# Kernel optimization log

Measured on AMD Instinct MI355X. Metric: run time of the kernel, lower is better.

The kernel has to match this reference:

```python
import jax, jax.numpy as jnp
import numpy as np

B, N = 2, 8192

PARAM_SHAPES = {
    'down0_w': (32, 3), 'down0_b': (32,),
    'sc1_w1': (32, 35), 'sc1_b1': (32,), 'sc1_w2': (64, 32), 'sc1_b2': (64,),
    'sc2_w1': (64, 67), 'sc2_b1': (64,), 'sc2_w2': (128, 64), 'sc2_b2': (128,),
    'sc3_w1': (128, 131), 'sc3_b1': (128,), 'sc3_w2': (192, 128), 'sc3_b2': (192,),
    'sc4_w1': (192, 195), 'sc4_b1': (192,), 'sc4_w2': (192, 192), 'sc4_b2': (192,),
    'up4_w1': (192, 195), 'up4_b1': (192,), 'up4_w2': (192, 384), 'up4_b2': (192,),
    'up3_w1': (128, 195), 'up3_b1': (128,), 'up3_w2': (128, 256), 'up3_b2': (128,),
    'up2_w1': (64, 131), 'up2_b1': (64,), 'up2_w2': (64, 128), 'up2_b2': (64,),
    'up1_w1': (32, 67), 'up1_b1': (32,), 'up1_w2': (32, 64), 'up1_b2': (32,),
}
PNAMES = list(PARAM_SHAPES.keys())


def _fps(xyz, m):
    # xyz [N,3] -> [m] int32 farthest-point-sample indices (deterministic, start at point 0)
    def body(dmin, _):
        nxt = jnp.argmax(dmin)
        d = jnp.sum((xyz - xyz[nxt]) ** 2, -1)
        return jnp.minimum(dmin, d), nxt.astype(jnp.int32)
    d0 = jnp.sum((xyz - xyz[0]) ** 2, -1)
    _, rest = jax.lax.scan(body, d0, None, length=m - 1)
    return jnp.concatenate([jnp.zeros((1,), jnp.int32), rest])


def _gather(pts, idx):
    # pts [B,N,C], idx [B,...] -> [B,...,C]
    return jax.vmap(lambda p, i: p[i])(pts, idx)


def _ball_query(new_xyz, xyz, radius, k):
    # first-k points within radius, invalid slots filled with the first valid index
    d2 = jnp.sum((new_xyz[:, :, None, :] - xyz[:, None, :, :]) ** 2, -1)  # [B,M,N]
    n = xyz.shape[1]
    order = jnp.where(d2 <= radius * radius, jnp.arange(n)[None, None, :], n)
    idx = jnp.argsort(order, axis=-1)[..., :k]
    valid = jnp.take_along_axis(order, idx, -1) < n
    return jnp.where(valid, idx, idx[..., :1])


def _knn(query, ref, k):
    d2 = jnp.sum((query[:, :, None, :] - ref[:, None, :, :]) ** 2, -1)  # [B,Nq,Nr]
    _, idx = jax.lax.top_k(-d2, k)
    return idx


def _mlp(h, w, b):
    # pointwise shared MLP layer with ReLU on channel-last tensor
    return jax.nn.relu(jnp.einsum('...c,oc->...o', h, w) + b)


def _set_conv(xyz, feat, npoint, radius, k, w1, b1, w2, b2):
    # PointNet++-style SetConv: FPS -> ball-query group -> shared MLP -> max-pool
    fps_idx = jax.vmap(_fps, (0, None))(xyz, npoint)          # [B,M]
    new_xyz = _gather(xyz, fps_idx)                            # [B,M,3]
    gi = _ball_query(new_xyz, xyz, radius, k)                  # [B,M,k]
    h = jnp.concatenate([_gather(xyz, gi) - new_xyz[:, :, None, :], _gather(feat, gi)], -1)
    h = _mlp(_mlp(h, w1, b1), w2, b2)                          # [B,M,k,Cout]
    return new_xyz, fps_idx, jnp.max(h, axis=2)


def _set_upconv(s_xyz, d_xyz, s_feat, d_feat, k, w1, b1, w2, b2):
    # FlowNet3D-style SetUpConv: kNN from dense to sparse -> MLP -> max-pool -> fuse with dense feat
    gi = _knn(d_xyz, s_xyz, k)                                 # [B,Nd,k]
    h = jnp.concatenate([_gather(s_xyz, gi) - d_xyz[:, :, None, :], _gather(s_feat, gi)], -1)
    pooled = jnp.max(_mlp(h, w1, b1), axis=2)                  # [B,Nd,m1]
    return _mlp(jnp.concatenate([pooled, d_feat], -1), w2, b2)


def _encoder(pc, feat, p):
    xyz = jnp.transpose(pc, (0, 2, 1))                         # [B,N,3]
    f0 = _mlp(jnp.transpose(feat, (0, 2, 1)), p['down0_w'], p['down0_b'])  # [B,N,32]
    xyz1, i1, f1 = _set_conv(xyz, f0, 2048, 0.5, 16, p['sc1_w1'], p['sc1_b1'], p['sc1_w2'], p['sc1_b2'])
    xyz2, i2, f2 = _set_conv(xyz1, f1, 512, 1.0, 16, p['sc2_w1'], p['sc2_b1'], p['sc2_w2'], p['sc2_b2'])
    xyz3, i3, f3 = _set_conv(xyz2, f2, 128, 2.0, 16, p['sc3_w1'], p['sc3_b1'], p['sc3_w2'], p['sc3_b2'])
    xyz4, i4, f4 = _set_conv(xyz3, f3, 64, 4.0, 16, p['sc4_w1'], p['sc4_b1'], p['sc4_w2'], p['sc4_b2'])
    u3 = _set_upconv(xyz4, xyz3, f4, f3, 8, p['up4_w1'], p['up4_b1'], p['up4_w2'], p['up4_b2'])
    u2 = _set_upconv(xyz3, xyz2, u3, f2, 8, p['up3_w1'], p['up3_b1'], p['up3_w2'], p['up3_b2'])
    u1 = _set_upconv(xyz2, xyz1, u2, f1, 8, p['up2_w1'], p['up2_b1'], p['up2_w2'], p['up2_b2'])
    u0 = _set_upconv(xyz1, xyz, u1, f0, 8, p['up1_w1'], p['up1_b1'], p['up1_w2'], p['up1_b2'])
    return (xyz1, xyz2, xyz3), (i1, i2, i3), (u0, u1, u2, u3)


def setup_inputs() -> dict:
    key = jax.random.key(0)
    ks = jax.random.split(key, 2 + len(PNAMES))
    inp = {
        'pc': jax.random.normal(ks[0], (B, 3, N), jnp.float32),
        'feat': jax.random.normal(ks[1], (B, 3, N), jnp.float32),
    }
    for i, name in enumerate(PNAMES):
        inp[name] = jax.random.normal(ks[2 + i], PARAM_SHAPES[name], jnp.float32) * 0.05
    return inp


def reference(pc, feat, down0_w, down0_b, sc1_w1, sc1_b1, sc1_w2, sc1_b2, sc2_w1, sc2_b1, sc2_w2, sc2_b2, sc3_w1, sc3_b1, sc3_w2, sc3_b2, sc4_w1, sc4_b1, sc4_w2, sc4_b2, up4_w1, up4_b1, up4_w2, up4_b2, up3_w1, up3_b1, up3_w2, up3_b2, up2_w1, up2_b1, up2_w2, up2_b2, up1_w1, up1_b1, up1_w2, up1_b2):
    # GenFlow_unit.forward with gts[0] is None -> pure encoder path
    loc = locals()
    p = {k: loc[k] for k in PNAMES}
    (x1, x2, x3), (i1, i2, i3), (u0, u1, u2, u3) = _encoder(pc, feat, p)
    t = lambda a: jnp.transpose(a, (0, 2, 1))  # back to torch channel-first convention
    return (t(x1), t(x2), t(x3), i1, i2, i3, t(u0), t(u1), t(u2), t(u3))
```

## Files before the change

### kernel.cpp

```cpp
#include <hip/hip_runtime.h>
#include <hip/hip_bf16.h>
#include <cstdint>

#define DEV __device__ __forceinline__

typedef float f32x2 __attribute__((ext_vector_type(2)));

DEV float sqdist(float ax, float ay, float az, float bx, float by, float bz) {
    float dx = __fsub_rn(ax, bx), dy = __fsub_rn(ay, by), dz = __fsub_rn(az, bz);
    return __fadd_rn(__fadd_rn(__fmul_rn(dx, dx), __fmul_rn(dy, dy)), __fmul_rn(dz, dz));
}

DEV f32x2 sqdist2(f32x2 ax, f32x2 ay, f32x2 az, float bx, float by, float bz) {
#pragma clang fp contract(off)
    f32x2 dx = ax - bx, dy = ay - by, dz = az - bz;
    return (dx * dx + dy * dy) + dz * dz;
}

DEV unsigned short f2bf(float f) {
    unsigned int u = __float_as_uint(f);
    u += 0x7fffu + ((u >> 16) & 1u);
    return (unsigned short)(u >> 16);
}

DEV float bf2f(unsigned short u) { return __uint_as_float(((unsigned int)u) << 16); }

template <int CTRL>
DEV int dpp_i(int v) { return __builtin_amdgcn_update_dpp(v, v, CTRL, 0xf, 0xf, false); }
template <int CTRL>
DEV float dpp_f(float v) { return __int_as_float(dpp_i<CTRL>(__float_as_int(v))); }

enum : int {
    O_X1 = 0, O_X2 = 12288, O_X3 = 15360,
    O_I1 = 16128, O_I2 = 20224, O_I3 = 21248,
    O_U0 = 21504, O_U1 = 545792, O_U2 = 807936, O_U3 = 939008
};

__global__ __launch_bounds__(256) void k_init(const float* __restrict__ pc,
                                              const float* __restrict__ feat,
                                              const float* __restrict__ w0,
                                              const float* __restrict__ b0,
                                              float* __restrict__ xyz,
                                              unsigned short* __restrict__ f0) {
    const int N = 8192;
    int i = blockIdx.x * blockDim.x + threadIdx.x;
    if (i >= 2 * N) return;
    int b = i / N, n = i % N;
    float fx0 = feat[(b * 3 + 0) * N + n];
    float fx1 = feat[(b * 3 + 1) * N + n];
    float fx2 = feat[(b * 3 + 2) * N + n];
    xyz[i * 3 + 0] = pc[(b * 3 + 0) * N + n];
    xyz[i * 3 + 1] = pc[(b * 3 + 1) * N + n];
    xyz[i * 3 + 2] = pc[(b * 3 + 2) * N + n];
#pragma unroll
    for (int o = 0; o < 32; o++) {
        float acc = b0[o];
        acc = fmaf(w0[o * 3 + 0], fx0, acc);
        acc = fmaf(w0[o * 3 + 1], fx1, acc);
        acc = fmaf(w0[o * 3 + 2], fx2, acc);
        f0[(size_t)i * 32 + o] = f2bf(fmaxf(acc, 0.f));
    }
}

template <int N, int M, int T>
DEV void fps_body(int b, int t, const float* __restrict__ xyz,
                  int* __restrict__ idx_out, char* smem) {
    constexpr int P = N / T;
    constexpr int P2 = P / 2;
    constexpr int W = T / 64;
    const float* X = xyz + (size_t)b * N * 3;
    float* sx = (float*)smem;
    float* sy = sx + N;
    float* sz = sy + N;
    unsigned long long* skey = (unsigned long long*)(smem + 12 * N);
    f32x2 px[P2], py[P2], pz[P2], dmin[P2];
    float c0x = X[0], c0y = X[1], c0z = X[2];
#pragma unroll
    for (int i = 0; i < P2; i++) {
        int p0 = (2 * i) * T + t, p1 = (2 * i + 1) * T + t;
        px[i] = f32x2{X[p0 * 3 + 0], X[p1 * 3 + 0]};
        py[i] = f32x2{X[p0 * 3 + 1], X[p1 * 3 + 1]};
        pz[i] = f32x2{X[p0 * 3 + 2], X[p1 * 3 + 2]};
        sx[p0] = px[i].x; sy[p0] = py[i].x; sz[p0] = pz[i].x;
        sx[p1] = px[i].y; sy[p1] = py[i].y; sz[p1] = pz[i].y;
        dmin[i] = sqdist2(px[i], py[i], pz[i], c0x, c0y, c0z);
    }
    if (t == 0) {
        idx_out[b * M] = 0;
        skey[0] = 0; skey[1] = 0; skey[2] = 0;
    }
    __syncthreads();
    int jm = 1;
    for (int j = 1; j < M; j++) {
        f32x2 m2[P2];
#pragma unroll
        for (int i = 0; i < P2; i++) m2[i] = dmin[i];
#pragma unroll
        for (int s = P2 / 2; s >= 1; s >>= 1)
#pragma unroll
            for (int i = 0; i < s; i++) m2[i] = __builtin_elementwise_max(m2[i], m2[i + s]);
        float bv = fmaxf(m2[0].x, m2[0].y);
        int ii[P];
#pragma unroll
        for (int i = 0; i < P; i++)
            ii[i] = (dmin[i >> 1][i & 1] == bv) ? (i * T + t) : 0x7fffffff;
#pragma unroll
        for (int s = P / 2; s >= 1; s >>= 1)
#pragma unroll
            for (int i = 0; i < s; i++) ii[i] = min(ii[i], ii[i + s]);
        int bi = ii[0];
        float bw = bv;
        bw = fmaxf(bw, dpp_f<0x121>(bw));
        bw = fmaxf(bw, dpp_f<0x122>(bw));
        bw = fmaxf(bw, dpp_f<0x124>(bw));
        bw = fmaxf(bw, dpp_f<0x128>(bw));
        bw = fmaxf(bw, dpp_f<0x142>(bw));
        bw = fmaxf(bw, dpp_f<0x143>(bw));
        float bvw = __int_as_float(__builtin_amdgcn_readlane(__float_as_int(bw), 63));
        unsigned int im = (bv == bvw) ? (unsigned int)bi : 0xffffffffu;
        im = min(im, (unsigned int)dpp_i<0x121>((int)im));
        im = min(im, (unsigned int)dpp_i<0x122>((int)im));
        im = min(im, (unsigned int)dpp_i<0x124>((int)im));
        im = min(im, (unsigned int)dpp_i<0x128>((int)im));
        im = min(im, (unsigned int)dpp_i<0x142>((int)im));
        im = min(im, (unsigned int)dpp_i<0x143>((int)im));
        int biw = __builtin_amdgcn_readlane((int)im, 63);
        int gi;
        if constexpr (W > 1) {
            unsigned long long key =
                ((unsigned long long)__float_as_uint(bvw) << 32) | (unsigned int)~biw;
            if ((t & 63) == 0) atomicMax(&skey[jm], key);
            __syncthreads();
            unsigned long long gk = skey[jm];
            gi = (int)~(unsigned int)gk;
            if (t == 0) skey[jm == 0 ? 2 : jm - 1] = 0;
            jm = (jm == 2) ? 0 : jm + 1;
        } else {
            gi = biw;
        }
        if (t == 0) idx_out[b * M + j] = gi;
        float cx = sx[gi], cy = sy[gi], cz = sz[gi];
#pragma unroll
        for (int i = 0; i < P2; i++)
            dmin[i] = __builtin_elementwise_min(
                dmin[i], sqdist2(px[i], py[i], pz[i], cx, cy, cz));
    }
}

template <int N, int M, int T>
__global__ __launch_bounds__(T, 1) void k_fps(const float* __restrict__ xyz,
                                              int* __restrict__ idx_out) {
    __shared__ __align__(16) char smem[12 * N + 24];
    fps_body<N, M, T>(blockIdx.x, threadIdx.x, xyz, idx_out, smem);
}

__global__ __launch_bounds__(256) void k_gather(const float* __restrict__ xyz_src,
                                                const int* __restrict__ idx,
                                                float* __restrict__ xyz_dst,
                                                int NS, int M) {
    int i = blockIdx.x * blockDim.x + threadIdx.x;
    if (i >= 2 * M) return;
    int b = i / M;
    int id = idx[i] & (NS - 1);
    xyz_dst[i * 3 + 0] = xyz_src[((size_t)b * NS + id) * 3 + 0];
    xyz_dst[i * 3 + 1] = xyz_src[((size_t)b * NS + id) * 3 + 1];
    xyz_dst[i * 3 + 2] = xyz_src[((size_t)b * NS + id) * 3 + 2];
}

template <int NS, int CF, int CMID, int COUT>
DEV void setconv_body(int q, int bb, int tid, int bdim,
                      const float* __restrict__ X, const unsigned short* __restrict__ F,
                      const float* __restrict__ C, const float* __restrict__ w1,
                      const float* __restrict__ b1, const float* __restrict__ w2,
                      const float* __restrict__ b2, unsigned short* __restrict__ fout,
                      float r2, int M, char* smem) {
    constexpr int CIN = 3 + CF;
    constexpr int K = 16;
    constexpr int M8 = CMID / 8;
    constexpr int O8 = COUT / 8;
    int blk = bb * M + q;
    const float* Xb = X + (size_t)bb * NS * 3;
    const unsigned short* Fb = F + (size_t)bb * NS * CF;
    int* s_n = (int*)smem;
    int* s_cntp = (int*)(smem + 64);
    float* s_h = (float*)(smem + 80);
    float* s_mid = s_h + K * CIN;
    float* s_pool = s_mid + K * CMID;
    float cx = C[(size_t)blk * 3 + 0], cy = C[(size_t)blk * 3 + 1], cz = C[(size_t)blk * 3 + 2];
    if (tid < 64) {
        int lane = tid;
        int cnt = 0;
        for (int base = 0; base < NS; base += 64) {
            int p = base + lane;
            float d2 = sqdist(Xb[p * 3], Xb[p * 3 + 1], Xb[p * 3 + 2], cx, cy, cz);
            bool in = (d2 <= r2);
            unsigned long long msk = __ballot(in);
            if (in) {
                int pos = cnt + __popcll(msk & ((1ull << lane) - 1ull));
                if (pos < K) s_n[pos] = p;
            }
            cnt += __popcll(msk);
            if (cnt >= K) break;
        }
        if (lane == 0) *s_cntp = cnt < K ? cnt : K;
    }
    __syncthreads();
    int cnt = *s_cntp;
    if (tid >= cnt && tid < K) s_n[tid] = s_n[0];
    __syncthreads();
    for (int tIdx = tid; tIdx < K * CIN; tIdx += bdim) {
        int n = tIdx / CIN, c = tIdx % CIN;
        int gi = s_n[n];
        float v;
        if (c < 3) v = __fsub_rn(Xb[gi * 3 + c], (c == 0 ? cx : (c == 1 ? cy : cz)));
        else v = bf2f(Fb[(size_t)gi * CF + (c - 3)]);
        s_h[n * CIN + c] = v;
    }
    __syncthreads();
    if (tid < 128) {
        int n = tid >> 3, sub = tid & 7;
#pragma unroll
        for (int j = 0; j < M8; j++) {
            int m = sub * M8 + j;
            float acc = b1[m];
#pragma unroll 4
            for (int c = 0; c < CIN; c++) acc = fmaf(w1[m * CIN + c], s_h[n * CIN + c], acc);
            s_mid[n * CMID + m] = fmaxf(acc, 0.f);
        }
    }
    __syncthreads();
    if (tid < 128) {
        int n = tid >> 3, sub = tid & 7;
        float vals[O8];
#pragma unroll
        for (int j = 0; j < O8; j++) {
            int o = sub * O8 + j;
            float acc = b2[o];
#pragma unroll 4
            for (int c = 0; c < CMID; c++) acc = fmaf(w2[o * CMID + c], s_mid[n * CMID + c], acc);
            vals[j] = fmaxf(acc, 0.f);
        }
#pragma unroll
        for (int j = 0; j < O8; j++) {
            vals[j] = fmaxf(vals[j], __shfl_xor(vals[j], 8, 64));
            vals[j] = fmaxf(vals[j], __shfl_xor(vals[j], 16, 64));
            vals[j] = fmaxf(vals[j], __shfl_xor(vals[j], 32, 64));
        }
        int lw = tid & 63, wv = tid >> 6;
        if (lw < 8) {
#pragma unroll
            for (int j = 0; j < O8; j++) s_pool[wv * COUT + lw * O8 + j] = vals[j];
        }
    }
    __syncthreads();
    if (tid < 8) {
#pragma unroll
        for (int j = 0; j < O8; j++) {
            int o = tid * O8 + j;
            fout[(size_t)blk * COUT + o] = f2bf(fmaxf(s_pool[o], s_pool[COUT + o]));
        }
    }
}

template <int NS, int CF, int CMID, int COUT>
__global__ __launch_bounds__(128) void k_setconv(
    const float* __restrict__ X, const unsigned short* __restrict__ F,
    const float* __restrict__ C, const float* __restrict__ w1,
    const float* __restrict__ b1, const float* __restrict__ w2,
    const float* __restrict__ b2, unsigned short* __restrict__ fout,
    float r2, int M) {
    constexpr int K = 16;
    constexpr int CIN = 3 + CF;
    __shared__ __align__(16) char smem[80 + 4 * (K * CIN + K * CMID + 2 * COUT)];
    setconv_body<NS, CF, CMID, COUT>(blockIdx.x, blockIdx.y, threadIdx.x, blockDim.x,
                                     X, F, C, w1, b1, w2, b2, fout, r2, M, smem);
}

template <int N, int M, int T, int NS, int CF, int CMID, int COUT>
__global__ __launch_bounds__(T, 1) void k_fps_sc(
    const float* __restrict__ fxyz, int* __restrict__ idx_out,
    const float* __restrict__ X, const unsigned short* __restrict__ F,
    const float* __restrict__ C, const float* __restrict__ w1,
    const float* __restrict__ b1, const float* __restrict__ w2,
    const float* __restrict__ b2, unsigned short* __restrict__ fout,
    float r2, int Msc) {
    constexpr int K = 16;
    constexpr int CIN = 3 + CF;
    constexpr int FPS_B = 12 * N + 24;
    constexpr int SC_B = 80 + 4 * (K * CIN + K * CMID + 2 * COUT);
    constexpr int SB = FPS_B > SC_B ? FPS_B : SC_B;
    __shared__ __align__(16) char smem[SB];
    if (blockIdx.x < 2) {
        fps_body<N, M, T>(blockIdx.x, threadIdx.x, fxyz, idx_out, smem);
    } else {
        int lin = blockIdx.x - 2;
        int q = lin % Msc, bb = lin / Msc;
        setconv_body<NS, CF, CMID, COUT>(q, bb, threadIdx.x, blockDim.x,
                                         X, F, C, w1, b1, w2, b2, fout, r2, Msc, smem);
    }
}

template <int S, int CS, int CMID, int CD, int COUT, bool TRANS>
__global__ __launch_bounds__(64) void k_upconv(
    const float* __restrict__ SX, const float* __restrict__ DX,
    const void* __restrict__ SFv, const unsigned short* __restrict__ DF,
    const float* __restrict__ w1, const float* __restrict__ b1,
    const float* __restrict__ w2, const float* __restrict__ b2,
    float* __restrict__ out, int o_off, int ND) {
    constexpr int K = 8;
    constexpr int CIN = 3 + CS;
    constexpr int CIN2 = CMID + CD;
    constexpr int M8 = CMID / 8;
    int q = blockIdx.x, b = blockIdx.y;
    int blk = b * ND + q;
    int lane = threadIdx.x;
    const float* SXb = SX + (size_t)b * S * 3;
    float qx = DX[(size_t)blk * 3], qy = DX[(size_t)blk * 3 + 1], qz = DX[(size_t)blk * 3 + 2];
    __shared__ int s_k[K];
    __shared__ float s_h[K][CIN];
    __shared__ float s_in2[CIN2];
    float bd[K];
    int bi[K];
#pragma unroll
    for (int i = 0; i < K; i++) { bd[i] = 3.0e38f; bi[i] = 0x7fffffff; }
    for (int p = lane; p < S; p += 64) {
        float d2 = sqdist(SXb[p * 3], SXb[p * 3 + 1], SXb[p * 3 + 2], qx, qy, qz);
        if (d2 < bd[K - 1] || (d2 == bd[K - 1] && p < bi[K - 1])) {
            bd[K - 1] = d2; bi[K - 1] = p;
#pragma unroll
            for (int j = K - 1; j > 0; j--) {
                bool sw = (bd[j] < bd[j - 1]) || (bd[j] == bd[j - 1] && bi[j] < bi[j - 1]);
                if (sw) {
                    float tv = bd[j]; bd[j] = bd[j - 1]; bd[j - 1] = tv;
                    int ti = bi[j]; bi[j] = bi[j - 1]; bi[j - 1] = ti;
                }
            }
        }
    }
    for (int r = 0; r < K; r++) {
        float vv = bd[0];
        float bw = vv;
        bw = fminf(bw, dpp_f<0x121>(bw));
        bw = fminf(bw, dpp_f<0x122>(bw));
        bw = fminf(bw, dpp_f<0x124>(bw));
        bw = fminf(bw, dpp_f<0x128>(bw));
        bw = fminf(bw, dpp_f<0x142>(bw));
        bw = fminf(bw, dpp_f<0x143>(bw));
        float vw = __int_as_float(__builtin_amdgcn_readlane(__float_as_int(bw), 63));
        unsigned int im = (vv == vw) ? (unsigned int)bi[0] : 0xffffffffu;
        im = min(im, (unsigned int)dpp_i<0x121>((int)im));
        im = min(im, (unsigned int)dpp_i<0x122>((int)im));
        im = min(im, (unsigned int)dpp_i<0x124>((int)im));
        im = min(im, (unsigned int)dpp_i<0x128>((int)im));
        im = min(im, (unsigned int)dpp_i<0x142>((int)im));
        im = min(im, (unsigned int)dpp_i<0x143>((int)im));
        int iw = __builtin_amdgcn_readlane((int)im, 63);
        if (lane == 0) s_k[r] = iw;
        if (iw == bi[0]) {
#pragma unroll
            for (int j = 0; j < K - 1; j++) { bd[j] = bd[j + 1]; bi[j] = bi[j + 1]; }
            bd[K - 1] = 3.0e38f; bi[K - 1] = 0x7fffffff;
        }
    }
    __syncthreads();
    for (int tIdx = lane; tIdx < K * CIN; tIdx += 64) {
        int n = tIdx / CIN, c = tIdx % CIN;
        int gi = s_k[n];
        float v;
        if (c < 3) v = __fsub_rn(SXb[gi * 3 + c], (c == 0 ? qx : (c == 1 ? qy : qz)));
        else if (TRANS) v = ((const float*)SFv)[((size_t)b * CS + (c - 3)) * S + gi];
        else v = bf2f(((const unsigned short*)SFv)[((size_t)b * S + gi) * CS + (c - 3)]);
        s_h[n][c] = v;
    }
    for (int c = lane; c < CD; c += 64) s_in2[CMID + c] = bf2f(DF[(size_t)blk * CD + c]);
    __syncthreads();
    int n = lane >> 3, sub = lane & 7;
    float vals[M8];
#pragma unroll
    for (int j = 0; j < M8; j++) {
        int m = sub * M8 + j;
        float acc = b1[m];
#pragma unroll 4
        for (int c = 0; c < CIN; c++) acc = fmaf(w1[m * CIN + c], s_h[n][c], acc);
        vals[j] = fmaxf(acc, 0.f);
    }
#pragma unroll
    for (int j = 0; j < M8; j++) {
        vals[j] = fmaxf(vals[j], __shfl_xor(vals[j], 8, 64));
        vals[j] = fmaxf(vals[j], __shfl_xor(vals[j], 16, 64));
        vals[j] = fmaxf(vals[j], __shfl_xor(vals[j], 32, 64));
    }
    if (lane < 8) {
#pragma unroll
        for (int j = 0; j < M8; j++) s_in2[lane * M8 + j] = vals[j];
    }
    __syncthreads();
    for (int o = lane; o < COUT; o += 64) {
        float acc = b2[o];
#pragma unroll 4
        for (int c = 0; c < CIN2; c++) acc = fmaf(w2[o * CIN2 + c], s_in2[c], acc);
        out[o_off + ((size_t)b * COUT + o) * ND + q] = fmaxf(acc, 0.f);
    }
}

__global__ __launch_bounds__(256) void k_finalize(
    const float* __restrict__ xyz1, const float* __restrict__ xyz2,
    const float* __restrict__ xyz3, const int* __restrict__ idx1,
    const int* __restrict__ idx2, const int* __restrict__ idx3,
    float* __restrict__ out) {
    int i = blockIdx.x * blockDim.x + threadIdx.x;
    const float* xs;
    const int* is;
    int M, ox, oi, j;
    if (i < 4096) { xs = xyz1; is = idx1; M = 2048; ox = O_X1; oi = O_I1; j = i; }
    else if (i < 5120) { xs = xyz2; is = idx2; M = 512; ox = O_X2; oi = O_I2; j = i - 4096; }
    else if (i < 5376) { xs = xyz3; is = idx3; M = 128; ox = O_X3; oi = O_I3; j = i - 5120; }
    else return;
    int b = j / M, m = j % M;
    out[ox + (b * 3 + 0) * M + m] = xs[j * 3 + 0];
    out[ox + (b * 3 + 1) * M + m] = xs[j * 3 + 1];
    out[ox + (b * 3 + 2) * M + m] = xs[j * 3 + 2];
    out[oi + j] = (float)is[j];
}

extern "C" void kernel_launch(void* const* d_in, const int* in_sizes, int n_in,
                              void* d_out, int out_size, void* d_ws, size_t ws_size,
                              hipStream_t stream) {
    const float* pc = (const float*)d_in[0];
    const float* feat = (const float*)d_in[1];
    const float* w0 = (const float*)d_in[2];
    const float* b0v = (const float*)d_in[3];
    const float* sc1w1 = (const float*)d_in[4];  const float* sc1b1 = (const float*)d_in[5];
    const float* sc1w2 = (const float*)d_in[6];  const float* sc1b2 = (const float*)d_in[7];
    const float* sc2w1 = (const float*)d_in[8];  const float* sc2b1 = (const float*)d_in[9];
    const float* sc2w2 = (const float*)d_in[10]; const float* sc2b2 = (const float*)d_in[11];
    const float* sc3w1 = (const float*)d_in[12]; const float* sc3b1 = (const float*)d_in[13];
    const float* sc3w2 = (const float*)d_in[14]; const float* sc3b2 = (const float*)d_in[15];
    const float* sc4w1 = (const float*)d_in[16]; const float* sc4b1 = (const float*)d_in[17];
    const float* sc4w2 = (const float*)d_in[18]; const float* sc4b2 = (const float*)d_in[19];
    const float* up4w1 = (const float*)d_in[20]; const float* up4b1 = (const float*)d_in[21];
    const float* up4w2 = (const float*)d_in[22]; const float* up4b2 = (const float*)d_in[23];
    const float* up3w1 = (const float*)d_in[24]; const float* up3b1 = (const float*)d_in[25];
    const float* up3w2 = (const float*)d_in[26]; const float* up3b2 = (const float*)d_in[27];
    const float* up2w1 = (const float*)d_in[28]; const float* up2b1 = (const float*)d_in[29];
    const float* up2w2 = (const float*)d_in[30]; const float* up2b2 = (const float*)d_in[31];
    const float* up1w1 = (const float*)d_in[32]; const float* up1b1 = (const float*)d_in[33];
    const float* up1w2 = (const float*)d_in[34]; const float* up1b2 = (const float*)d_in[35];
    float* out = (float*)d_out;

    char* ws = (char*)d_ws;
    size_t off = 0;
    auto A = [&](size_t bytes) -> char* {
        char* p = ws + off;
        off += (bytes + 255) & ~(size_t)255;
        return p;
    };
    float* xyz  = (float*)A((size_t)2 * 8192 * 3 * 4);
    int* idx1   = (int*)A((size_t)2 * 2048 * 4);
    int* idx2   = (int*)A((size_t)2 * 512 * 4);
    int* idx3   = (int*)A((size_t)2 * 128 * 4);
    int* idx4   = (int*)A((size_t)2 * 64 * 4);
    float* xyz1 = (float*)A((size_t)2 * 2048 * 3 * 4);
    float* xyz2 = (float*)A((size_t)2 * 512 * 3 * 4);
    float* xyz3 = (float*)A((size_t)2 * 128 * 3 * 4);
    float* xyz4 = (float*)A((size_t)2 * 64 * 3 * 4);
    unsigned short* f0 = (unsigned short*)A((size_t)2 * 8192 * 32 * 2);
    unsigned short* f1 = (unsigned short*)A((size_t)2 * 2048 * 64 * 2);
    unsigned short* f2 = (unsigned short*)A((size_t)2 * 512 * 128 * 2);
    unsigned short* f3 = (unsigned short*)A((size_t)2 * 128 * 192 * 2);
    unsigned short* f4 = (unsigned short*)A((size_t)2 * 64 * 192 * 2);

    k_init<<<(2 * 8192 + 255) / 256, 256, 0, stream>>>(pc, feat, w0, b0v, xyz, f0);

    k_fps<8192, 2048, 512><<<2, 512, 0, stream>>>(xyz, idx1);
    k_gather<<<16, 256, 0, stream>>>(xyz, idx1, xyz1, 8192, 2048);
    k_fps_sc<2048, 512, 512, 8192, 32, 32, 64><<<2 + 2 * 2048, 512, 0, stream>>>(
        xyz1, idx2, xyz, f0, xyz1, sc1w1, sc1b1, sc1w2, sc1b2, f1, 0.25f, 2048);
    k_gather<<<4, 256, 0, stream>>>(xyz1, idx2, xyz2, 2048, 512);
    k_fps_sc<512, 128, 256, 2048, 64, 64, 128><<<2 + 2 * 512, 256, 0, stream>>>(
        xyz2, idx3, xyz1, f1, xyz2, sc2w1, sc2b1, sc2w2, sc2b2, f2, 1.0f, 512);
    k_gather<<<1, 256, 0, stream>>>(xyz2, idx3, xyz3, 512, 128);
    k_fps<128, 64, 64><<<2, 64, 0, stream>>>(xyz3, idx4);
    k_gather<<<1, 128, 0, stream>>>(xyz3, idx4, xyz4, 128, 64);
    k_setconv<512, 128, 128, 192><<<dim3(128, 2), 128, 0, stream>>>(
        xyz2, f2, xyz3, sc3w1, sc3b1, sc3w2, sc3b2, f3, 4.0f, 128);
    k_setconv<128, 192, 192, 192><<<dim3(64, 2), 128, 0, stream>>>(
        xyz3, f3, xyz4, sc4w1, sc4b1, sc4w2, sc4b2, f4, 16.0f, 64);

    k_upconv<64, 192, 192, 192, 192, false><<<dim3(128, 2), 64, 0, stream>>>(
        xyz4, xyz3, f4, f3, up4w1, up4b1, up4w2, up4b2, out, O_U3, 128);
    k_upconv<128, 192, 128, 128, 128, true><<<dim3(512, 2), 64, 0, stream>>>(
        xyz3, xyz2, out + O_U3, f2, up3w1, up3b1, up3w2, up3b2, out, O_U2, 512);
    k_upconv<512, 128, 64, 64, 64, true><<<dim3(2048, 2), 64, 0, stream>>>(
        xyz2, xyz1, out + O_U2, f1, up2w1, up2b1, up2w2, up2b2, out, O_U1, 2048);
    k_upconv<2048, 64, 32, 32, 32, true><<<dim3(8192, 2), 64, 0, stream>>>(
        xyz1, xyz, out + O_U1, f0, up1w1, up1b1, up1w2, up1b2, out, O_U0, 8192);

    k_finalize<<<(5376 + 255) / 256, 256, 0, stream>>>(
        xyz1, xyz2, xyz3, idx1, idx2, idx3, out);
}
```

Measured before the change: 3.846 ms.

## Spatially bin points and prune first-level FPS updates with per-thread bounding boxes

```diff
diff --git a/kernel.cpp b/kernel.cpp
--- a/kernel.cpp
+++ b/kernel.cpp
@@ -59,6 +59,181 @@
         acc = fmaf(w0[o * 3 + 1], fx1, acc);
         acc = fmaf(w0[o * 3 + 2], fx2, acc);
         f0[(size_t)i * 32 + o] = f2bf(fmaxf(acc, 0.f));
+    }
+}
+
+template <int N, int T>
+__global__ __launch_bounds__(T) void k_bin(const float* __restrict__ xyz,
+                                           float* __restrict__ xp, float* __restrict__ yp,
+                                           float* __restrict__ zp, int* __restrict__ pid) {
+    constexpr int W = T / 64;
+    int b = blockIdx.x, t = threadIdx.x;
+    const float* X = xyz + (size_t)b * N * 3;
+    __shared__ float smn[3][W], smx[3][W];
+    __shared__ int hist[512], scan[512], cnt[512];
+    float mn[3] = {3e38f, 3e38f, 3e38f}, mx[3] = {-3e38f, -3e38f, -3e38f};
+    for (int p = t; p < N; p += T) {
+        float v[3] = {X[p * 3], X[p * 3 + 1], X[p * 3 + 2]};
+#pragma unroll
+        for (int a = 0; a < 3; a++) { mn[a] = fminf(mn[a], v[a]); mx[a] = fmaxf(mx[a], v[a]); }
+    }
+#pragma unroll
+    for (int a = 0; a < 3; a++) {
+#pragma unroll
+        for (int m = 1; m < 64; m <<= 1) {
+            mn[a] = fminf(mn[a], __shfl_xor(mn[a], m, 64));
+            mx[a] = fmaxf(mx[a], __shfl_xor(mx[a], m, 64));
+        }
+    }
+    if ((t & 63) == 0) {
+#pragma unroll
+        for (int a = 0; a < 3; a++) { smn[a][t >> 6] = mn[a]; smx[a][t >> 6] = mx[a]; }
+    }
+    for (int i = t; i < 512; i += T) { hist[i] = 0; cnt[i] = 0; }
+    __syncthreads();
+#pragma unroll
+    for (int a = 0; a < 3; a++) {
+        mn[a] = smn[a][0]; mx[a] = smx[a][0];
+#pragma unroll
+        for (int w = 1; w < W; w++) { mn[a] = fminf(mn[a], smn[a][w]); mx[a] = fmaxf(mx[a], smx[a][w]); }
+    }
+    float inv[3];
+#pragma unroll
+    for (int a = 0; a < 3; a++) inv[a] = 8.0f / fmaxf(mx[a] - mn[a], 1e-9f);
+    auto bin_of = [&](float x, float y, float z) {
+        int ix = min(7, max(0, (int)((x - mn[0]) * inv[0])));
+        int iy = min(7, max(0, (int)((y - mn[1]) * inv[1])));
+        int iz = min(7, max(0, (int)((z - mn[2]) * inv[2])));
+        return (ix << 6) | (iy << 3) | iz;
+    };
+    for (int p = t; p < N; p += T) {
+        atomicAdd(&hist[bin_of(X[p * 3], X[p * 3 + 1], X[p * 3 + 2])], 1);
+    }
+    __syncthreads();
+    if (t < 512) scan[t] = hist[t];
+    __syncthreads();
+    for (int s = 1; s < 512; s <<= 1) {
+        int v = 0;
+        if (t < 512 && t >= s) v = scan[t - s];
+        __syncthreads();
+        if (t < 512) scan[t] += v;
+        __syncthreads();
+    }
+    for (int p = t; p < N; p += T) {
+        float x = X[p * 3], y = X[p * 3 + 1], z = X[p * 3 + 2];
+        int bid = bin_of(x, y, z);
+        int pos = (scan[bid] - hist[bid]) + atomicAdd(&cnt[bid], 1);
+        xp[(size_t)b * N + pos] = x;
+        yp[(size_t)b * N + pos] = y;
+        zp[(size_t)b * N + pos] = z;
+        pid[(size_t)b * N + pos] = p;
+    }
+}
+
+template <int N, int M, int T>
+__global__ __launch_bounds__(T, 1) void k_fps_pruned(
+    const float* __restrict__ xp, const float* __restrict__ yp,
+    const float* __restrict__ zp, const int* __restrict__ pidg,
+    const float* __restrict__ xyz, int* __restrict__ idx_out) {
+    constexpr int P = N / T;
+    constexpr int P2 = P / 2;
+    int b = blockIdx.x, t = threadIdx.x;
+    const float* XP = xp + (size_t)b * N;
+    const float* YP = yp + (size_t)b * N;
+    const float* ZP = zp + (size_t)b * N;
+    const int* PIDG = pidg + (size_t)b * N;
+    __shared__ float sx[N], sy[N], sz[N];
+    __shared__ int spid[N];
+    __shared__ unsigned long long skey[3];
+    f32x2 px[P2], py[P2], pz[P2], dmin[P2];
+    float c0x = xyz[(size_t)b * N * 3 + 0];
+    float c0y = xyz[(size_t)b * N * 3 + 1];
+    float c0z = xyz[(size_t)b * N * 3 + 2];
+    int base = t * P;
+    float blx = 3e38f, bly = 3e38f, blz = 3e38f, bhx = -3e38f, bhy = -3e38f, bhz = -3e38f;
+#pragma unroll
+    for (int i = 0; i < P2; i++) {
+        int p0 = base + 2 * i, p1 = p0 + 1;
+        px[i] = f32x2{XP[p0], XP[p1]};
+        py[i] = f32x2{YP[p0], YP[p1]};
+        pz[i] = f32x2{ZP[p0], ZP[p1]};
+        sx[p0] = px[i].x; sy[p0] = py[i].x; sz[p0] = pz[i].x;
+        sx[p1] = px[i].y; sy[p1] = py[i].y; sz[p1] = pz[i].y;
+        spid[p0] = PIDG[p0]; spid[p1] = PIDG[p1];
+        blx = fminf(blx, fminf(px[i].x, px[i].y)); bhx = fmaxf(bhx, fmaxf(px[i].x, px[i].y));
+        bly = fminf(bly, fminf(py[i].x, py[i].y)); bhy = fmaxf(bhy, fmaxf(py[i].x, py[i].y));
+        blz = fminf(blz, fminf(pz[i].x, pz[i].y)); bhz = fmaxf(bhz, fmaxf(pz[i].x, pz[i].y));
+        dmin[i] = sqdist2(px[i], py[i], pz[i], c0x, c0y, c0z);
+    }
+    if (t == 0) {
+        idx_out[b * M] = 0;
+        skey[0] = 0; skey[1] = 0; skey[2] = 0;
+    }
+    float bv;
+    int bi;
+    auto local_argmax = [&]() {
+        f32x2 m2[P2];
+#pragma unroll
+        for (int i = 0; i < P2; i++) m2[i] = dmin[i];
+#pragma unroll
+        for (int s = P2 / 2; s >= 1; s >>= 1)
+#pragma unroll
+            for (int i = 0; i < s; i++) m2[i] = __builtin_elementwise_max(m2[i], m2[i + s]);
+        bv = fmaxf(m2[0].x, m2[0].y);
+        int ii[P];
+#pragma unroll
+        for (int i = 0; i < P; i++)
+            ii[i] = (dmin[i >> 1][i & 1] == bv) ? (base + i) : 0x7fffffff;
+#pragma unroll
+        for (int s = P / 2; s >= 1; s >>= 1)
+#pragma unroll
+            for (int i = 0; i < s; i++) ii[i] = min(ii[i], ii[i + s]);
+        bi = ii[0];
+    };
+    local_argmax();
+    __syncthreads();
+    int jm = 1;
+    for (int j = 1; j < M; j++) {
+        float bw = bv;
+        bw = fmaxf(bw, dpp_f<0x121>(bw));
+        bw = fmaxf(bw, dpp_f<0x122>(bw));
+        bw = fmaxf(bw, dpp_f<0x124>(bw));
+        bw = fmaxf(bw, dpp_f<0x128>(bw));
+        bw = fmaxf(bw, dpp_f<0x142>(bw));
+        bw = fmaxf(bw, dpp_f<0x143>(bw));
+        float bvw = __int_as_float(__builtin_amdgcn_readlane(__float_as_int(bw), 63));
+        unsigned int im = (bv == bvw) ? (unsigned int)bi : 0xffffffffu;
+        im = min(im, (unsigned int)dpp_i<0x121>((int)im));
+        im = min(im, (unsigned int)dpp_i<0x122>((int)im));
+        im = min(im, (unsigned int)dpp_i<0x124>((int)im));
+        im = min(im, (unsigned int)dpp_i<0x128>((int)im));
+        im = min(im, (unsigned int)dpp_i<0x142>((int)im));
+        im = min(im, (unsigned int)dpp_i<0x143>((int)im));
+        int biw = __builtin_amdgcn_readlane((int)im, 63);
+        unsigned long long key =
+            ((unsigned long long)__float_as_uint(bvw) << 32) | (unsigned int)~biw;
+        if ((t & 63) == 0) atomicMax(&skey[jm], key);
+        __syncthreads();
+        unsigned long long gk = skey[jm];
+        int gi = (int)~(unsigned int)gk;
+        if (t == 0) {
+            idx_out[b * M + j] = spid[gi];
+            skey[jm == 0 ? 2 : jm - 1] = 0;
+        }
+        jm = (jm == 2) ? 0 : jm + 1;
+        float cx = sx[gi], cy = sy[gi], cz = sz[gi];
+        float qx = fminf(fmaxf(cx, blx), bhx);
+        float qy = fminf(fmaxf(cy, bly), bhy);
+        float qz = fminf(fmaxf(cz, blz), bhz);
+        float dxb = cx - qx, dyb = cy - qy, dzb = cz - qz;
+        float db = dxb * dxb + dyb * dyb + dzb * dzb;
+        if (!(db * 0.999f > bv)) {
+#pragma unroll
+            for (int i = 0; i < P2; i++)
+                dmin[i] = __builtin_elementwise_min(
+                    dmin[i], sqdist2(px[i], py[i], pz[i], cx, cy, cz));
+            local_argmax();
+        }
     }
 }
 
@@ -469,10 +644,15 @@
     unsigned short* f2 = (unsigned short*)A((size_t)2 * 512 * 128 * 2);
     unsigned short* f3 = (unsigned short*)A((size_t)2 * 128 * 192 * 2);
     unsigned short* f4 = (unsigned short*)A((size_t)2 * 64 * 192 * 2);
+    float* xp  = (float*)A((size_t)2 * 8192 * 4);
+    float* yp  = (float*)A((size_t)2 * 8192 * 4);
+    float* zp  = (float*)A((size_t)2 * 8192 * 4);
+    int* pid   = (int*)A((size_t)2 * 8192 * 4);
 
     k_init<<<(2 * 8192 + 255) / 256, 256, 0, stream>>>(pc, feat, w0, b0v, xyz, f0);
 
-    k_fps<8192, 2048, 512><<<2, 512, 0, stream>>>(xyz, idx1);
+    k_bin<8192, 512><<<2, 512, 0, stream>>>(xyz, xp, yp, zp, pid);
+    k_fps_pruned<8192, 2048, 512><<<2, 512, 0, stream>>>(xp, yp, zp, pid, xyz, idx1);
     k_gather<<<16, 256, 0, stream>>>(xyz, idx1, xyz1, 8192, 2048);
     k_fps_sc<2048, 512, 512, 8192, 32, 32, 64><<<2 + 2 * 2048, 512, 0, stream>>>(
         xyz1, idx2, xyz, f0, xyz1, sc1w1, sc1b1, sc1w2, sc1b2, f1, 0.25f, 2048);
```

Result: faster. 3.660 ms (-4.9%).
